# Performance work log

Measured on AMD Instinct MI355X. Metric: run time of the kernel, lower is better.

The kernel has to match this reference:

```python
import jax, jax.numpy as jnp
import numpy as np

B, N, N_IN, N_HID, EIN = 8, 256, 64, 128, 16


def setup_inputs() -> dict:
    key = jax.random.key(0)
    ks = jax.random.split(key, 12)
    s_in = 1.0 / np.sqrt(N_IN)
    s_e = 1.0 / np.sqrt(EIN)
    s_h = 1.0 / np.sqrt(N_HID)
    return {
        "x": jax.random.normal(ks[0], (B, N, N_IN), jnp.float32),
        "e": jax.random.normal(ks[1], (B, N, N, EIN), jnp.float32),
        "Wf": jax.random.uniform(ks[2], (N_IN, N_HID), jnp.float32, -s_in, s_in),
        "bf": jax.random.uniform(ks[3], (N_HID,), jnp.float32, -s_in, s_in),
        "Wt": jax.random.uniform(ks[4], (N_IN, N_HID), jnp.float32, -s_in, s_in),
        "bt": jax.random.uniform(ks[5], (N_HID,), jnp.float32, -s_in, s_in),
        "We": jax.random.uniform(ks[6], (EIN, N_HID), jnp.float32, -s_e, s_e),
        "be": jax.random.uniform(ks[7], (N_HID,), jnp.float32, -s_e, s_e),
        "W1": jax.random.uniform(ks[8], (N_HID, N_HID), jnp.float32, -s_h, s_h),
        "b1": jax.random.uniform(ks[9], (N_HID,), jnp.float32, -s_h, s_h),
        "W2": jax.random.uniform(ks[10], (N_HID, N_IN), jnp.float32, -s_h, s_h),
        "b2": jax.random.uniform(ks[11], (N_IN,), jnp.float32, -s_h, s_h),
    }


def reference(x, e, Wf, bf, Wt, bt, We, be, W1, b1, W2, b2):
    # x: [B,N,F], e: [B,N,N,E]
    n = x.shape[1]
    ne_f = x @ Wf + bf                      # [B,N,H] (node_emb_1)
    ne_t = x @ Wt + bt                      # [B,N,H] (node_emb_2)
    ee = e @ We + be                        # [B,N,N,H]
    # pair[b,i,j] = node_emb_1[b,j] + node_emb_2[b,i] + edge_emb[b,i,j]
    pair = ne_f[:, None, :, :] + ne_t[:, :, None, :] + ee
    # zero the diagonal (both node_emb and edge_emb diagonals were zeroed)
    mask = (1.0 - jnp.eye(n, dtype=x.dtype))[None, :, :, None]
    node_emb = jax.nn.relu(pair * mask).mean(axis=2)  # [B,N,H]
    h = jax.nn.relu(node_emb @ W1 + b1)
    return h @ W2 + b2 + x
```

## Files before the change

### kernel.cpp

```cpp
#include <hip/hip_runtime.h>
#include <hip/hip_bf16.h>


#define BB 8
#define NN 256
#define FF 64
#define HH 128
#define EE 16
#define NCH 5

typedef __attribute__((ext_vector_type(8))) short bf16x8;
typedef __attribute__((ext_vector_type(16))) float f32x16;

__device__ __forceinline__ short f2bf(float f) {
    union { float f; unsigned u; } v; v.f = f;
    unsigned r = v.u + 0x7FFFu + ((v.u >> 16) & 1u);
    return (short)(r >> 16);
}
__device__ __forceinline__ float bf2f(short s) {
    union { unsigned u; float f; } v; v.u = ((unsigned)(unsigned short)s) << 16;
    return v.f;
}
__device__ __forceinline__ unsigned pkbf(float lo, float hi) {
    unsigned r;
    asm("v_cvt_pk_bf16_f32 %0, %1, %2" : "=v"(r) : "v"(lo), "v"(hi));
    return r;
}
union bfu { bf16x8 v; unsigned u[4]; };

__global__ __launch_bounds__(128) void k_prep(
    const float* __restrict__ x, const float* __restrict__ Wt,
    const float* __restrict__ bf, const float* __restrict__ bt, const float* __restrict__ be,
    const float* __restrict__ We, const float* __restrict__ Wf,
    const float* __restrict__ W1, const float* __restrict__ W2,
    float* __restrict__ net, short* __restrict__ xbf, short* __restrict__ xbfp,
    short* __restrict__ Bpack, short* __restrict__ W1p, short* __restrict__ W2p)
{
    __shared__ float smx[4 * FF];
    const int tid = threadIdx.x;
    const int row0 = blockIdx.x * 4;

    smx[tid]       = x[(size_t)row0 * FF + tid];
    smx[tid + 128] = x[(size_t)row0 * FF + tid + 128];
    __syncthreads();

    const int h = tid;
    const float bsum = bf[h] + bt[h] + be[h];
    float a0 = bsum, a1 = bsum, a2 = bsum, a3 = bsum;

    #pragma unroll 8
    for (int k = 0; k < FF; ++k) {
        const float wt = Wt[k * HH + h];
        a0 = fmaf(smx[k], wt, a0);
        a1 = fmaf(smx[FF + k], wt, a1);
        a2 = fmaf(smx[2 * FF + k], wt, a2);
        a3 = fmaf(smx[3 * FF + k], wt, a3);
    }
    net[(size_t)(row0 + 0) * HH + h] = a0;
    net[(size_t)(row0 + 1) * HH + h] = a1;
    net[(size_t)(row0 + 2) * HH + h] = a2;
    net[(size_t)(row0 + 3) * HH + h] = a3;

    {
        const int r = tid >> 6, f = tid & 63;
        xbf[(size_t)(row0 + r) * FF + f]     = f2bf(smx[r * FF + f]);
        xbf[(size_t)(row0 + r + 2) * FF + f] = f2bf(smx[(r + 2) * FF + f]);
    }

    {
        const int r    = tid >> 5;
        const int q    = tid & 31;
        const int ch   = q >> 3;
        const int half = (q >> 2) & 1;
        const int el2  = q & 3;
        const int gj   = row0 + r;
        const int bb   = gj >> 8;
        const int jj   = gj & 255;
        const int jt   = jj >> 5;
        const int cc   = jj & 31;
        const float lo = smx[r * FF + ch * 16 + half * 8 + el2 * 2];
        const float hi = smx[r * FF + ch * 16 + half * 8 + el2 * 2 + 1];
        ((unsigned*)xbfp)[((((size_t)bb * 8 + jt) * 4 + ch) * 64 + half * 32 + cc) * 4 + el2]
            = pkbf(lo, hi);
    }

    if (blockIdx.x < 32) {
        for (int t = blockIdx.x * 128 + tid; t < 34816; t += 32 * 128) {
            if (t < 10240) {
                const int el = t & 7, lane = (t >> 3) & 63, ht = (t >> 9) & 3, ch = t >> 11;
                const int kl = 8 * (lane >> 5) + el;
                const int hh = ht * 32 + (lane & 31);
                Bpack[t] = f2bf(ch == 0 ? We[kl * HH + hh] : Wf[(16 * (ch - 1) + kl) * HH + hh]);
            } else if (t < 26624) {
                const int t2 = t - 10240;
                const int el = t2 & 7, lane = (t2 >> 3) & 63, ht = (t2 >> 9) & 3, ch = (t2 >> 11) & 7;
                const int k = 16 * ch + 8 * (lane >> 5) + el;
                const int hh = ht * 32 + (lane & 31);
                W1p[t2] = f2bf(W1[k * HH + hh]);
            } else {
                const int t3 = t - 26624;
                const int el = t3 & 7, lane = (t3 >> 3) & 63, ht = (t3 >> 9) & 1, ch = t3 >> 10;
                const int k = 16 * ch + 8 * (lane >> 5) + el;
                const int hh = ht * 32 + (lane & 31);
                W2p[t3] = f2bf(W2[k * FF + hh]);
            }
        }
    }
}

__global__ __launch_bounds__(256) void k_pair(
    const float* __restrict__ e, const float* __restrict__ net,
    const short* __restrict__ xbfp, const short* __restrict__ Bpack,
    float* __restrict__ S)
{
    const int row  = blockIdx.x;
    const int b    = row >> 8;
    const int tid  = threadIdx.x;
    const int wave = tid >> 6;
    const int lane = tid & 63;
    const int c    = lane & 31;
    const int half = lane >> 5;

    __shared__ __align__(16) char eL[8 * 1024];

    const bf16x8* __restrict__ bp = (const bf16x8*)Bpack;
    bf16x8 bfrag[NCH];
    #pragma unroll
    for (int ch = 0; ch < NCH; ++ch)
        bfrag[ch] = bp[(ch * 4 + wave) * 64 + lane];

    const float netv = net[(size_t)row * HH + wave * 32 + c];

    const float* __restrict__ eRow = e + (size_t)row * (NN * EE);
    const bf16x8* __restrict__ xq  = (const bf16x8*)(xbfp + (size_t)b * 8 * 4 * 512);

    const int sc   = tid >> 3;
    const int sk2  = tid & 7;
    const int edst = ((sk2 >> 2) * 128 + sc * 4 + (sk2 & 3)) * 4;

    #pragma unroll
    for (int jt = 0; jt < 8; ++jt) {
        const float2 ev = *(const float2*)(eRow + (size_t)jt * 512 + tid * 2);
        *(unsigned*)(&eL[jt * 1024 + edst]) = pkbf(ev.x, ev.y);
    }
    __syncthreads();

    float acc0 = 0.f, acc1 = 0.f, acc2 = 0.f, acc3 = 0.f;

    #pragma unroll
    for (int jt = 0; jt < 8; ++jt) {
        const bf16x8 ae  = *(const bf16x8*)(&eL[jt * 1024 + half * 512 + c * 16]);
        const bf16x8 ax0 = xq[((size_t)jt * 4 + 0) * 64 + lane];
        const bf16x8 ax1 = xq[((size_t)jt * 4 + 1) * 64 + lane];
        const bf16x8 ax2 = xq[((size_t)jt * 4 + 2) * 64 + lane];
        const bf16x8 ax3 = xq[((size_t)jt * 4 + 3) * 64 + lane];

        f32x16 d = {netv,netv,netv,netv, netv,netv,netv,netv,
                    netv,netv,netv,netv, netv,netv,netv,netv};
        d = __builtin_amdgcn_mfma_f32_32x32x16_bf16(ae,  bfrag[0], d, 0, 0, 0);
        d = __builtin_amdgcn_mfma_f32_32x32x16_bf16(ax0, bfrag[1], d, 0, 0, 0);
        d = __builtin_amdgcn_mfma_f32_32x32x16_bf16(ax1, bfrag[2], d, 0, 0, 0);
        d = __builtin_amdgcn_mfma_f32_32x32x16_bf16(ax2, bfrag[3], d, 0, 0, 0);
        d = __builtin_amdgcn_mfma_f32_32x32x16_bf16(ax3, bfrag[4], d, 0, 0, 0);

        #pragma unroll
        for (int r = 0; r < 16; r += 4) {
            acc0 += fmaxf(d[r + 0], 0.f);
            acc1 += fmaxf(d[r + 1], 0.f);
            acc2 += fmaxf(d[r + 2], 0.f);
            acc3 += fmaxf(d[r + 3], 0.f);
        }
    }

    float acc = (acc0 + acc1) + (acc2 + acc3);
    acc += __shfl_xor(acc, 32);
    if (lane < 32) S[(size_t)row * HH + wave * 32 + c] = acc;
}

__global__ __launch_bounds__(256) void k_mlp(
    const float* __restrict__ x, const float* __restrict__ e,
    const float* __restrict__ S, const float* __restrict__ net,
    const short* __restrict__ xbf, const short* __restrict__ Bpack,
    const short* __restrict__ W1p, const short* __restrict__ W2p,
    const float* __restrict__ b1, const float* __restrict__ b2,
    float* __restrict__ out)
{
    const int row0 = blockIdx.x * 32;
    const int tid  = threadIdx.x;
    const int wave = tid >> 6;
    const int lane = tid & 63;
    const int c    = lane & 31;
    const int half = lane >> 5;

    __shared__ float Dt[32][132];
    __shared__ short neL[32][136];
    __shared__ short h1L[32][136];

    {
        const int gr = row0 + c;
        const int bb = gr >> 8, ii = gr & (NN - 1);
        const float* ed = e + ((size_t)(bb * NN + ii) * NN + ii) * EE + 8 * half;
        const float4 p0 = ((const float4*)ed)[0];
        const float4 p1 = ((const float4*)ed)[1];
        bfu ae;
        ae.u[0] = pkbf(p0.x, p0.y);
        ae.u[1] = pkbf(p0.z, p0.w);
        ae.u[2] = pkbf(p1.x, p1.y);
        ae.u[3] = pkbf(p1.z, p1.w);

        const bf16x8* xp = (const bf16x8*)(xbf + (size_t)gr * FF + 8 * half);
        const bf16x8 ax0 = xp[0];
        const bf16x8 ax1 = xp[2];
        const bf16x8 ax2 = xp[4];
        const bf16x8 ax3 = xp[6];

        const bf16x8* bp = (const bf16x8*)Bpack;
        f32x16 d = {0.f,0.f,0.f,0.f, 0.f,0.f,0.f,0.f, 0.f,0.f,0.f,0.f, 0.f,0.f,0.f,0.f};
        d = __builtin_amdgcn_mfma_f32_32x32x16_bf16(ae.v, bp[(0*4+wave)*64+lane], d, 0, 0, 0);
        d = __builtin_amdgcn_mfma_f32_32x32x16_bf16(ax0,  bp[(1*4+wave)*64+lane], d, 0, 0, 0);
        d = __builtin_amdgcn_mfma_f32_32x32x16_bf16(ax1,  bp[(2*4+wave)*64+lane], d, 0, 0, 0);
        d = __builtin_amdgcn_mfma_f32_32x32x16_bf16(ax2,  bp[(3*4+wave)*64+lane], d, 0, 0, 0);
        d = __builtin_amdgcn_mfma_f32_32x32x16_bf16(ax3,  bp[(4*4+wave)*64+lane], d, 0, 0, 0);
        #pragma unroll
        for (int r = 0; r < 16; ++r) {
            const int rowj = (r & 3) + 8 * (r >> 2) + 4 * half;
            Dt[rowj][wave * 32 + c] = d[r];
        }
    }
    __syncthreads();

    {
        const int r  = tid >> 3;
        const int h0 = (tid & 7) * 16;
        const size_t base = (size_t)(row0 + r) * HH + h0;
        unsigned uo[8];
        #pragma unroll
        for (int q = 0; q < 4; ++q) {
            const float4 sv = *(const float4*)&S[base + 4 * q];
            const float4 nv = *(const float4*)&net[base + 4 * q];
            const float4 dv = *(const float4*)&Dt[r][h0 + 4 * q];
            const float n0 = (sv.x - fmaxf(dv.x + nv.x, 0.f)) * (1.0f / NN);
            const float n1 = (sv.y - fmaxf(dv.y + nv.y, 0.f)) * (1.0f / NN);
            const float n2 = (sv.z - fmaxf(dv.z + nv.z, 0.f)) * (1.0f / NN);
            const float n3 = (sv.w - fmaxf(dv.w + nv.w, 0.f)) * (1.0f / NN);
            uo[2 * q]     = pkbf(n0, n1);
            uo[2 * q + 1] = pkbf(n2, n3);
        }
        uint4* dst = (uint4*)&neL[r][h0];
        dst[0] = make_uint4(uo[0], uo[1], uo[2], uo[3]);
        dst[1] = make_uint4(uo[4], uo[5], uo[6], uo[7]);
    }
    __syncthreads();

    {
        const float b1v = b1[wave * 32 + c];
        const bf16x8* wp = (const bf16x8*)W1p;
        f32x16 d = {b1v,b1v,b1v,b1v, b1v,b1v,b1v,b1v, b1v,b1v,b1v,b1v, b1v,b1v,b1v,b1v};
        #pragma unroll
        for (int ch = 0; ch < 8; ++ch) {
            const bf16x8 a = *(const bf16x8*)&neL[c][16 * ch + 8 * half];
            d = __builtin_amdgcn_mfma_f32_32x32x16_bf16(a, wp[(ch * 4 + wave) * 64 + lane], d, 0, 0, 0);
        }
        #pragma unroll
        for (int r = 0; r < 16; ++r) {
            const int rowj = (r & 3) + 8 * (r >> 2) + 4 * half;
            h1L[rowj][wave * 32 + c] = f2bf(fmaxf(d[r], 0.f));
        }
    }
    __syncthreads();

    if (wave < 2) {
        const float b2v = b2[wave * 32 + c];
        const bf16x8* wp = (const bf16x8*)W2p;
        f32x16 d = {b2v,b2v,b2v,b2v, b2v,b2v,b2v,b2v, b2v,b2v,b2v,b2v, b2v,b2v,b2v,b2v};
        #pragma unroll
        for (int ch = 0; ch < 8; ++ch) {
            const bf16x8 a = *(const bf16x8*)&h1L[c][16 * ch + 8 * half];
            d = __builtin_amdgcn_mfma_f32_32x32x16_bf16(a, wp[(ch * 2 + wave) * 64 + lane], d, 0, 0, 0);
        }
        #pragma unroll
        for (int r = 0; r < 16; ++r) {
            const int rowj = (r & 3) + 8 * (r >> 2) + 4 * half;
            const size_t idx = (size_t)(row0 + rowj) * FF + wave * 32 + c;
            out[idx] = d[r] + x[idx];
        }
    }
}

extern "C" void kernel_launch(void* const* d_in, const int* in_sizes, int n_in,
                              void* d_out, int out_size, void* d_ws, size_t ws_size,
                              hipStream_t stream) {
    (void)in_sizes; (void)n_in; (void)out_size; (void)ws_size;
    const float* x  = (const float*)d_in[0];
    const float* e  = (const float*)d_in[1];
    const float* Wf = (const float*)d_in[2];
    const float* bf = (const float*)d_in[3];
    const float* Wt = (const float*)d_in[4];
    const float* bt = (const float*)d_in[5];
    const float* We = (const float*)d_in[6];
    const float* be = (const float*)d_in[7];
    const float* W1 = (const float*)d_in[8];
    const float* b1 = (const float*)d_in[9];
    const float* W2 = (const float*)d_in[10];
    const float* b2 = (const float*)d_in[11];
    float* out = (float*)d_out;

    char* w = (char*)d_ws;
    float* net   = (float*)w;                 w += (size_t)BB * NN * HH * 4;
    float* Sbuf  = (float*)w;                 w += (size_t)BB * NN * HH * 4;
    short* xbf   = (short*)w;                 w += (size_t)BB * NN * FF * 2;
    short* xbfp  = (short*)w;                 w += (size_t)BB * NN * FF * 2;
    short* Bpack = (short*)w;                 w += NCH * 4 * 64 * 8 * 2;
    short* W1p   = (short*)w;                 w += 8 * 4 * 64 * 8 * 2;
    short* W2p   = (short*)w;

    k_prep<<<(BB * NN) / 4, 128, 0, stream>>>(x, Wt, bf, bt, be, We, Wf, W1, W2,
                                              net, xbf, xbfp, Bpack, W1p, W2p);
    k_pair<<<BB * NN, 256, 0, stream>>>(e, net, xbfp, Bpack, Sbuf);
    k_mlp<<<(BB * NN) / 32, 256, 0, stream>>>(x, e, Sbuf, net, xbf, Bpack, W1p, W2p,
                                              b1, b2, out);
}
```

Baseline: 119.0 us.

## Fold diagonal correction into pair kernel and stage x tiles in LDS

The pair kernel now picks the diagonal j==i term from its own MFMA output, subtracts relu of it, scales by 1/N and writes the node embedding as bf16. The MLP kernel therefore no longer recomputes the diagonal pair term or reads S, net, e and xbf, and the xbf buffer is gone. The pair kernel also copies the batch's packed x fragments (32 KB) into LDS once per block instead of reading them from global memory in the MFMA loop. The extra LDS and the select logic may lower occupancy of the pair kernel.

```diff
diff --git a/kernel.cpp b/kernel.cpp
--- a/kernel.cpp
+++ b/kernel.cpp
@@ -17,23 +17,18 @@
     unsigned r = v.u + 0x7FFFu + ((v.u >> 16) & 1u);
     return (short)(r >> 16);
 }
-__device__ __forceinline__ float bf2f(short s) {
-    union { unsigned u; float f; } v; v.u = ((unsigned)(unsigned short)s) << 16;
-    return v.f;
-}
 __device__ __forceinline__ unsigned pkbf(float lo, float hi) {
     unsigned r;
     asm("v_cvt_pk_bf16_f32 %0, %1, %2" : "=v"(r) : "v"(lo), "v"(hi));
     return r;
 }
-union bfu { bf16x8 v; unsigned u[4]; };
 
 __global__ __launch_bounds__(128) void k_prep(
     const float* __restrict__ x, const float* __restrict__ Wt,
     const float* __restrict__ bf, const float* __restrict__ bt, const float* __restrict__ be,
     const float* __restrict__ We, const float* __restrict__ Wf,
     const float* __restrict__ W1, const float* __restrict__ W2,
-    float* __restrict__ net, short* __restrict__ xbf, short* __restrict__ xbfp,
+    float* __restrict__ net, short* __restrict__ xbfp,
     short* __restrict__ Bpack, short* __restrict__ W1p, short* __restrict__ W2p)
 {
     __shared__ float smx[4 * FF];
@@ -60,12 +55,6 @@
     net[(size_t)(row0 + 1) * HH + h] = a1;
     net[(size_t)(row0 + 2) * HH + h] = a2;
     net[(size_t)(row0 + 3) * HH + h] = a3;
-
-    {
-        const int r = tid >> 6, f = tid & 63;
-        xbf[(size_t)(row0 + r) * FF + f]     = f2bf(smx[r * FF + f]);
-        xbf[(size_t)(row0 + r + 2) * FF + f] = f2bf(smx[(r + 2) * FF + f]);
-    }
 
     {
         const int r    = tid >> 5;
@@ -111,10 +100,11 @@
 __global__ __launch_bounds__(256) void k_pair(
     const float* __restrict__ e, const float* __restrict__ net,
     const short* __restrict__ xbfp, const short* __restrict__ Bpack,
-    float* __restrict__ S)
+    short* __restrict__ neb)
 {
     const int row  = blockIdx.x;
     const int b    = row >> 8;
+    const int i    = row & (NN - 1);
     const int tid  = threadIdx.x;
     const int wave = tid >> 6;
     const int lane = tid & 63;
@@ -122,6 +112,7 @@
     const int half = lane >> 5;
 
     __shared__ __align__(16) char eL[8 * 1024];
+    __shared__ __align__(16) char xL[32 * 1024];
 
     const bf16x8* __restrict__ bp = (const bf16x8*)Bpack;
     bf16x8 bfrag[NCH];
@@ -132,12 +123,15 @@
     const float netv = net[(size_t)row * HH + wave * 32 + c];
 
     const float* __restrict__ eRow = e + (size_t)row * (NN * EE);
-    const bf16x8* __restrict__ xq  = (const bf16x8*)(xbfp + (size_t)b * 8 * 4 * 512);
+    const uint4* __restrict__ xqg  = (const uint4*)(xbfp + (size_t)b * 8 * 4 * 512);
+
+    #pragma unroll
+    for (int k = 0; k < 8; ++k)
+        ((uint4*)xL)[k * 256 + tid] = xqg[k * 256 + tid];
 
     const int sc   = tid >> 3;
     const int sk2  = tid & 7;
     const int edst = ((sk2 >> 2) * 128 + sc * 4 + (sk2 & 3)) * 4;
-
     #pragma unroll
     for (int jt = 0; jt < 8; ++jt) {
         const float2 ev = *(const float2*)(eRow + (size_t)jt * 512 + tid * 2);
@@ -145,15 +139,22 @@
     }
     __syncthreads();
 
+    const int tloc     = i & 31;
+    const int jtstar   = i >> 5;
+    const int halfstar = (tloc >> 2) & 1;
+    const int rstar    = (tloc & 3) + 4 * (tloc >> 3);
+    float dgv = 0.f;
+
     float acc0 = 0.f, acc1 = 0.f, acc2 = 0.f, acc3 = 0.f;
+    const bf16x8* __restrict__ xf = (const bf16x8*)xL;
 
     #pragma unroll
     for (int jt = 0; jt < 8; ++jt) {
         const bf16x8 ae  = *(const bf16x8*)(&eL[jt * 1024 + half * 512 + c * 16]);
-        const bf16x8 ax0 = xq[((size_t)jt * 4 + 0) * 64 + lane];
-        const bf16x8 ax1 = xq[((size_t)jt * 4 + 1) * 64 + lane];
-        const bf16x8 ax2 = xq[((size_t)jt * 4 + 2) * 64 + lane];
-        const bf16x8 ax3 = xq[((size_t)jt * 4 + 3) * 64 + lane];
+        const bf16x8 ax0 = xf[(jt * 4 + 0) * 64 + lane];
+        const bf16x8 ax1 = xf[(jt * 4 + 1) * 64 + lane];
+        const bf16x8 ax2 = xf[(jt * 4 + 2) * 64 + lane];
+        const bf16x8 ax3 = xf[(jt * 4 + 3) * 64 + lane];
 
         f32x16 d = {netv,netv,netv,netv, netv,netv,netv,netv,
                     netv,netv,netv,netv, netv,netv,netv,netv};
@@ -163,6 +164,11 @@
         d = __builtin_amdgcn_mfma_f32_32x32x16_bf16(ax2, bfrag[3], d, 0, 0, 0);
         d = __builtin_amdgcn_mfma_f32_32x32x16_bf16(ax3, bfrag[4], d, 0, 0, 0);
 
+        if (jt == jtstar && half == halfstar) {
+            #pragma unroll
+            for (int r = 0; r < 16; ++r) dgv = (r == rstar) ? d[r] : dgv;
+        }
+
         #pragma unroll
         for (int r = 0; r < 16; r += 4) {
             acc0 += fmaxf(d[r + 0], 0.f);
@@ -173,14 +179,14 @@
     }
 
     float acc = (acc0 + acc1) + (acc2 + acc3);
+    acc -= fmaxf(dgv, 0.f);
     acc += __shfl_xor(acc, 32);
-    if (lane < 32) S[(size_t)row * HH + wave * 32 + c] = acc;
+    if (lane < 32)
+        neb[(size_t)row * HH + wave * 32 + c] = f2bf(acc * (1.0f / (float)NN));
 }
 
 __global__ __launch_bounds__(256) void k_mlp(
-    const float* __restrict__ x, const float* __restrict__ e,
-    const float* __restrict__ S, const float* __restrict__ net,
-    const short* __restrict__ xbf, const short* __restrict__ Bpack,
+    const float* __restrict__ x, const short* __restrict__ neb,
     const short* __restrict__ W1p, const short* __restrict__ W2p,
     const float* __restrict__ b1, const float* __restrict__ b2,
     float* __restrict__ out)
@@ -192,63 +198,16 @@
     const int c    = lane & 31;
     const int half = lane >> 5;
 
-    __shared__ float Dt[32][132];
     __shared__ short neL[32][136];
     __shared__ short h1L[32][136];
-
-    {
-        const int gr = row0 + c;
-        const int bb = gr >> 8, ii = gr & (NN - 1);
-        const float* ed = e + ((size_t)(bb * NN + ii) * NN + ii) * EE + 8 * half;
-        const float4 p0 = ((const float4*)ed)[0];
-        const float4 p1 = ((const float4*)ed)[1];
-        bfu ae;
-        ae.u[0] = pkbf(p0.x, p0.y);
-        ae.u[1] = pkbf(p0.z, p0.w);
-        ae.u[2] = pkbf(p1.x, p1.y);
-        ae.u[3] = pkbf(p1.z, p1.w);
-
-        const bf16x8* xp = (const bf16x8*)(xbf + (size_t)gr * FF + 8 * half);
-        const bf16x8 ax0 = xp[0];
-        const bf16x8 ax1 = xp[2];
-        const bf16x8 ax2 = xp[4];
-        const bf16x8 ax3 = xp[6];
-
-        const bf16x8* bp = (const bf16x8*)Bpack;
-        f32x16 d = {0.f,0.f,0.f,0.f, 0.f,0.f,0.f,0.f, 0.f,0.f,0.f,0.f, 0.f,0.f,0.f,0.f};
-        d = __builtin_amdgcn_mfma_f32_32x32x16_bf16(ae.v, bp[(0*4+wave)*64+lane], d, 0, 0, 0);
-        d = __builtin_amdgcn_mfma_f32_32x32x16_bf16(ax0,  bp[(1*4+wave)*64+lane], d, 0, 0, 0);
-        d = __builtin_amdgcn_mfma_f32_32x32x16_bf16(ax1,  bp[(2*4+wave)*64+lane], d, 0, 0, 0);
-        d = __builtin_amdgcn_mfma_f32_32x32x16_bf16(ax2,  bp[(3*4+wave)*64+lane], d, 0, 0, 0);
-        d = __builtin_amdgcn_mfma_f32_32x32x16_bf16(ax3,  bp[(4*4+wave)*64+lane], d, 0, 0, 0);
-        #pragma unroll
-        for (int r = 0; r < 16; ++r) {
-            const int rowj = (r & 3) + 8 * (r >> 2) + 4 * half;
-            Dt[rowj][wave * 32 + c] = d[r];
-        }
-    }
-    __syncthreads();
 
     {
         const int r  = tid >> 3;
         const int h0 = (tid & 7) * 16;
-        const size_t base = (size_t)(row0 + r) * HH + h0;
-        unsigned uo[8];
-        #pragma unroll
-        for (int q = 0; q < 4; ++q) {
-            const float4 sv = *(const float4*)&S[base + 4 * q];
-            const float4 nv = *(const float4*)&net[base + 4 * q];
-            const float4 dv = *(const float4*)&Dt[r][h0 + 4 * q];
-            const float n0 = (sv.x - fmaxf(dv.x + nv.x, 0.f)) * (1.0f / NN);
-            const float n1 = (sv.y - fmaxf(dv.y + nv.y, 0.f)) * (1.0f / NN);
-            const float n2 = (sv.z - fmaxf(dv.z + nv.z, 0.f)) * (1.0f / NN);
-            const float n3 = (sv.w - fmaxf(dv.w + nv.w, 0.f)) * (1.0f / NN);
-            uo[2 * q]     = pkbf(n0, n1);
-            uo[2 * q + 1] = pkbf(n2, n3);
-        }
+        const uint4* src = (const uint4*)&neb[(size_t)(row0 + r) * HH + h0];
         uint4* dst = (uint4*)&neL[r][h0];
-        dst[0] = make_uint4(uo[0], uo[1], uo[2], uo[3]);
-        dst[1] = make_uint4(uo[4], uo[5], uo[6], uo[7]);
+        dst[0] = src[0];
+        dst[1] = src[1];
     }
     __syncthreads();
 
@@ -307,16 +266,14 @@
 
     char* w = (char*)d_ws;
     float* net   = (float*)w;                 w += (size_t)BB * NN * HH * 4;
-    float* Sbuf  = (float*)w;                 w += (size_t)BB * NN * HH * 4;
-    short* xbf   = (short*)w;                 w += (size_t)BB * NN * FF * 2;
+    short* neb   = (short*)w;                 w += (size_t)BB * NN * HH * 2;
     short* xbfp  = (short*)w;                 w += (size_t)BB * NN * FF * 2;
     short* Bpack = (short*)w;                 w += NCH * 4 * 64 * 8 * 2;
     short* W1p   = (short*)w;                 w += 8 * 4 * 64 * 8 * 2;
     short* W2p   = (short*)w;
 
     k_prep<<<(BB * NN) / 4, 128, 0, stream>>>(x, Wt, bf, bt, be, We, Wf, W1, W2,
-                                              net, xbf, xbfp, Bpack, W1p, W2p);
-    k_pair<<<BB * NN, 256, 0, stream>>>(e, net, xbfp, Bpack, Sbuf);
-    k_mlp<<<(BB * NN) / 32, 256, 0, stream>>>(x, e, Sbuf, net, xbf, Bpack, W1p, W2p,
-                                              b1, b2, out);
-}
+                                              net, xbfp, Bpack, W1p, W2p);
+    k_pair<<<BB * NN, 256, 0, stream>>>(e, net, xbfp, Bpack, neb);
+    k_mlp<<<(BB * NN) / 32, 256, 0, stream>>>(x, neb, W1p, W2p, b1, b2, out);
+}
```

Result: slower. 121.5 us (+2.1%).
